# Kernel tuning notes

Hardware: AMD Instinct MI355X
Metric: run time of the kernel (lower is better)

Reference implementation:

```python
import jax, jax.numpy as jnp
import numpy as np

D_MODEL = 768
BOTTLENECK = 64
LN_EPS = 1e-5
SCALE = 1.0


def setup_inputs() -> dict:
    key = jax.random.key(0)
    k_x, k_wd = jax.random.split(key, 2)
    x = jax.random.normal(k_x, (8, 4096, D_MODEL), dtype=jnp.float32)
    # LayerNorm affine params
    ln_gamma = jnp.ones((D_MODEL,), dtype=jnp.float32)
    ln_beta = jnp.zeros((D_MODEL,), dtype=jnp.float32)
    # down_proj: kaiming_uniform_(a=sqrt(5)) -> bound = 1/sqrt(fan_in)
    bound = 1.0 / np.sqrt(D_MODEL)
    w_down = jax.random.uniform(k_wd, (D_MODEL, BOTTLENECK), dtype=jnp.float32,
                                minval=-bound, maxval=bound)
    b_down = jnp.zeros((BOTTLENECK,), dtype=jnp.float32)
    # up_proj initialized to zeros per 'lora' init; use small nonzero to make grads informative?
    # Stay faithful: zeros, as in the module's init.
    w_up = jnp.zeros((BOTTLENECK, D_MODEL), dtype=jnp.float32)
    b_up = jnp.zeros((D_MODEL,), dtype=jnp.float32)
    return {"x": x, "ln_gamma": ln_gamma, "ln_beta": ln_beta,
            "w_down": w_down, "b_down": b_down, "w_up": w_up, "b_up": b_up}


def _layer_norm(x, gamma, beta):
    mean = jnp.mean(x, axis=-1, keepdims=True)
    var = jnp.var(x, axis=-1, keepdims=True)
    return (x - mean) * jax.lax.rsqrt(var + LN_EPS) * gamma + beta


def reference(x, ln_gamma, ln_beta, w_down, b_down, w_up, b_up):
    # adapter_layernorm_option == 'in': LN before down projection
    h = _layer_norm(x, ln_gamma, ln_beta)              # [B, S, D]
    down = jnp.einsum('bsd,dk->bsk', h, w_down) + b_down  # [B, S, K]
    down = jax.nn.relu(down)
    # dropout is identity in eval mode
    out = jnp.einsum('bsk,kd->bsd', down, w_up) + b_up    # [B, S, D]
    return out * SCALE
```

## Files before the change

kernel.cpp:

```cpp
#include <hip/hip_runtime.h>
#include <hip/hip_bf16.h>


#define D_MODEL 768
#define KB      64
#define NTHR    256
#define PPAD    72

typedef __attribute__((ext_vector_type(8))) short    bf16x8;
typedef __attribute__((ext_vector_type(4))) float    f32x4;
typedef __attribute__((ext_vector_type(4))) unsigned short us4;

static __device__ __forceinline__ unsigned short f2bf(float f) {
  unsigned int u = __builtin_bit_cast(unsigned int, f);
  unsigned int r = u + 0x7FFFu + ((u >> 16) & 1u);
  return (unsigned short)(r >> 16);
}

__global__ void adapter_prep(const float* __restrict__ wd,
                             const float* __restrict__ wu,
                             const float* __restrict__ gamma,
                             const float* __restrict__ beta,
                             const float* __restrict__ bdown,
                             unsigned short* __restrict__ wdT,
                             unsigned short* __restrict__ wuT,
                             float* __restrict__ s_arr,
                             float* __restrict__ t_arr) {
  const int b = blockIdx.x;
  const int t = threadIdx.x;
  if (b < 192) {
    const int i = b * 256 + t;
    const int k1 = i / D_MODEL;
    const int d1 = i - k1 * D_MODEL;
    wdT[i] = f2bf(gamma[d1] * wd[(size_t)d1 * KB + k1]);
    const int d2 = i >> 6;
    const int k2 = i & 63;
    wuT[i] = f2bf(wu[(size_t)k2 * D_MODEL + d2]);
  } else {
    const int k = t & 63;
    const int c = t >> 6;
    float ss = 0.f, tt = 0.f;
    const int d0 = c * 192;
    #pragma unroll 4
    for (int d = d0; d < d0 + 192; ++d) {
      const float w = wd[(size_t)d * KB + k];
      ss = fmaf(gamma[d], w, ss);
      tt = fmaf(beta[d],  w, tt);
    }
    __shared__ float ps[4][64], pt[4][64];
    ps[c][k] = ss; pt[c][k] = tt;
    __syncthreads();
    if (t < 64) {
      s_arr[t] = ps[0][t] + ps[1][t] + ps[2][t] + ps[3][t];
      t_arr[t] = pt[0][t] + pt[1][t] + pt[2][t] + pt[3][t] + bdown[t];
    }
  }
}

__global__ void __launch_bounds__(NTHR, 4) adapter_main(
    const float* __restrict__ x,
    const float* __restrict__ s_arr,
    const float* __restrict__ t_arr,
    const unsigned short* __restrict__ wdT,
    const unsigned short* __restrict__ wuT,
    const float* __restrict__ b_up,
    float* __restrict__ out) {

  __shared__ unsigned short p_s[4][16][PPAD];

  const int t   = threadIdx.x;
  const int wid = t >> 6;
  const int l   = t & 63;
  const int lr  = l & 15;
  const int lg  = l >> 4;
  const int row0 = blockIdx.x * 64 + wid * 16;

  const float* xp = x + (size_t)(row0 + lr) * D_MODEL + 8 * lg;
  const unsigned short* wp = wdT + (size_t)lr * D_MODEL + 8 * lg;

  f32x4 acc0 = {0.f,0.f,0.f,0.f}, acc1 = {0.f,0.f,0.f,0.f};
  f32x4 acc2 = {0.f,0.f,0.f,0.f}, acc3 = {0.f,0.f,0.f,0.f};
  float s1 = 0.f, s2 = 0.f;

  #pragma unroll
  for (int kk = 0; kk < 24; ++kk) {
    const float4 v0 = *(const float4*)(xp + 32 * kk);
    const float4 v1 = *(const float4*)(xp + 32 * kk + 4);
    s1 += (v0.x + v0.y) + (v0.z + v0.w) + (v1.x + v1.y) + (v1.z + v1.w);
    s2 = fmaf(v0.x, v0.x, s2); s2 = fmaf(v0.y, v0.y, s2);
    s2 = fmaf(v0.z, v0.z, s2); s2 = fmaf(v0.w, v0.w, s2);
    s2 = fmaf(v1.x, v1.x, s2); s2 = fmaf(v1.y, v1.y, s2);
    s2 = fmaf(v1.z, v1.z, s2); s2 = fmaf(v1.w, v1.w, s2);
    bf16x8 xf;
    xf[0] = (short)f2bf(v0.x); xf[1] = (short)f2bf(v0.y);
    xf[2] = (short)f2bf(v0.z); xf[3] = (short)f2bf(v0.w);
    xf[4] = (short)f2bf(v1.x); xf[5] = (short)f2bf(v1.y);
    xf[6] = (short)f2bf(v1.z); xf[7] = (short)f2bf(v1.w);
    const bf16x8 wa0 = *(const bf16x8*)(wp + 32 * kk);
    const bf16x8 wa1 = *(const bf16x8*)(wp + 16 * D_MODEL + 32 * kk);
    const bf16x8 wa2 = *(const bf16x8*)(wp + 32 * D_MODEL + 32 * kk);
    const bf16x8 wa3 = *(const bf16x8*)(wp + 48 * D_MODEL + 32 * kk);
    acc0 = __builtin_amdgcn_mfma_f32_16x16x32_bf16(wa0, xf, acc0, 0, 0, 0);
    acc1 = __builtin_amdgcn_mfma_f32_16x16x32_bf16(wa1, xf, acc1, 0, 0, 0);
    acc2 = __builtin_amdgcn_mfma_f32_16x16x32_bf16(wa2, xf, acc2, 0, 0, 0);
    acc3 = __builtin_amdgcn_mfma_f32_16x16x32_bf16(wa3, xf, acc3, 0, 0, 0);
  }

  s1 += __shfl_xor(s1, 16); s1 += __shfl_xor(s1, 32);
  s2 += __shfl_xor(s2, 16); s2 += __shfl_xor(s2, 32);
  const float mu  = s1 * (1.0f / 768.0f);
  const float var = s2 * (1.0f / 768.0f) - mu * mu;
  const float rs  = rsqrtf(var + 1e-5f);
  const float nm  = -rs * mu;

  #pragma unroll
  for (int c = 0; c < 4; ++c) {
    const f32x4 a = (c == 0) ? acc0 : (c == 1) ? acc1 : (c == 2) ? acc2 : acc3;
    const float4 sv = *(const float4*)(s_arr + 16 * c + 4 * lg);
    const float4 tv = *(const float4*)(t_arr + 16 * c + 4 * lg);
    us4 pk;
    pk.x = f2bf(fmaxf(fmaf(rs, a[0], fmaf(nm, sv.x, tv.x)), 0.f));
    pk.y = f2bf(fmaxf(fmaf(rs, a[1], fmaf(nm, sv.y, tv.y)), 0.f));
    pk.z = f2bf(fmaxf(fmaf(rs, a[2], fmaf(nm, sv.z, tv.z)), 0.f));
    pk.w = f2bf(fmaxf(fmaf(rs, a[3], fmaf(nm, sv.w, tv.w)), 0.f));
    *(us4*)&p_s[wid][lr][16 * c + 4 * lg] = pk;
  }

  __syncthreads();

  const bf16x8 pa0 = *(const bf16x8*)&p_s[wid][lr][8 * lg];
  const bf16x8 pa1 = *(const bf16x8*)&p_s[wid][lr][32 + 8 * lg];
  float* op = out + (size_t)(row0 + 4 * lg) * D_MODEL + lr;

  #pragma unroll 4
  for (int n = 0; n < 48; ++n) {
    const int cn = 16 * n;
    const unsigned short* bp = wuT + (size_t)(cn + lr) * KB + 8 * lg;
    f32x4 c0 = {0.f, 0.f, 0.f, 0.f};
    c0 = __builtin_amdgcn_mfma_f32_16x16x32_bf16(pa0, *(const bf16x8*)(bp), c0, 0, 0, 0);
    c0 = __builtin_amdgcn_mfma_f32_16x16x32_bf16(pa1, *(const bf16x8*)(bp + 32), c0, 0, 0, 0);
    const float bu = b_up[cn + lr];
    op[(size_t)0 * D_MODEL + cn] = c0[0] + bu;
    op[(size_t)1 * D_MODEL + cn] = c0[1] + bu;
    op[(size_t)2 * D_MODEL + cn] = c0[2] + bu;
    op[(size_t)3 * D_MODEL + cn] = c0[3] + bu;
  }
}

extern "C" void kernel_launch(void* const* d_in, const int* in_sizes, int n_in,
                              void* d_out, int out_size, void* d_ws, size_t ws_size,
                              hipStream_t stream) {
  const float* x     = (const float*)d_in[0];
  const float* gamma = (const float*)d_in[1];
  const float* beta  = (const float*)d_in[2];
  const float* wd    = (const float*)d_in[3];
  const float* bdown = (const float*)d_in[4];
  const float* wu    = (const float*)d_in[5];
  const float* bup   = (const float*)d_in[6];
  float* out = (float*)d_out;

  char* ws = (char*)d_ws;
  unsigned short* wdT = (unsigned short*)ws;
  unsigned short* wuT = (unsigned short*)(ws + 98304);
  float* s_arr = (float*)(ws + 196608);
  float* t_arr = (float*)(ws + 196864);

  const int rows = in_sizes[0] / D_MODEL;

  adapter_prep<<<193, NTHR, 0, stream>>>(wd, wu, gamma, beta, bdown,
                                         wdT, wuT, s_arr, t_arr);
  adapter_main<<<rows / 64, NTHR, 0, stream>>>(x, s_arr, t_arr, wdT, wuT, bup, out);
}
```

Before: 224.5 us.

## Software-pipeline x and weight loads in adapter main kernel with register double buffering

The main kernel now prefetches x rows in chunks and the down-projection weight fragments two steps ahead into double-buffered registers. The up-projection weights and biases are likewise prefetched chunk by chunk, so global loads overlap with MFMA work. The unneeded block-wide __syncthreads is dropped because each wave reads only its own LDS slice. Launch bounds are relaxed to 2 waves per SIMD to make room for the extra registers, and the prep kernel is retiled to 1024-thread blocks, trading occupancy for memory-level parallelism within each wave.

```diff
diff --git a/kernel.cpp b/kernel.cpp
--- a/kernel.cpp
+++ b/kernel.cpp
@@ -7,6 +7,11 @@
 #define NTHR    256
 #define PPAD    72
 
+#define CH1     4
+#define NCH1    6
+#define CH2     6
+#define NCH2    8
+
 typedef __attribute__((ext_vector_type(8))) short    bf16x8;
 typedef __attribute__((ext_vector_type(4))) float    f32x4;
 typedef __attribute__((ext_vector_type(4))) unsigned short us4;
@@ -17,19 +22,20 @@
   return (unsigned short)(r >> 16);
 }
 
-__global__ void adapter_prep(const float* __restrict__ wd,
-                             const float* __restrict__ wu,
-                             const float* __restrict__ gamma,
-                             const float* __restrict__ beta,
-                             const float* __restrict__ bdown,
-                             unsigned short* __restrict__ wdT,
-                             unsigned short* __restrict__ wuT,
-                             float* __restrict__ s_arr,
-                             float* __restrict__ t_arr) {
+__global__ void __launch_bounds__(1024) adapter_prep(
+    const float* __restrict__ wd,
+    const float* __restrict__ wu,
+    const float* __restrict__ gamma,
+    const float* __restrict__ beta,
+    const float* __restrict__ bdown,
+    unsigned short* __restrict__ wdT,
+    unsigned short* __restrict__ wuT,
+    float* __restrict__ s_arr,
+    float* __restrict__ t_arr) {
   const int b = blockIdx.x;
   const int t = threadIdx.x;
-  if (b < 192) {
-    const int i = b * 256 + t;
+  if (b < 48) {
+    const int i = b * 1024 + t;
     const int k1 = i / D_MODEL;
     const int d1 = i - k1 * D_MODEL;
     wdT[i] = f2bf(gamma[d1] * wd[(size_t)d1 * KB + k1]);
@@ -40,24 +46,27 @@
     const int k = t & 63;
     const int c = t >> 6;
     float ss = 0.f, tt = 0.f;
-    const int d0 = c * 192;
+    const int d0 = c * 48;
     #pragma unroll 4
-    for (int d = d0; d < d0 + 192; ++d) {
+    for (int d = d0; d < d0 + 48; ++d) {
       const float w = wd[(size_t)d * KB + k];
       ss = fmaf(gamma[d], w, ss);
       tt = fmaf(beta[d],  w, tt);
     }
-    __shared__ float ps[4][64], pt[4][64];
+    __shared__ float ps[16][64], pt[16][64];
     ps[c][k] = ss; pt[c][k] = tt;
     __syncthreads();
     if (t < 64) {
-      s_arr[t] = ps[0][t] + ps[1][t] + ps[2][t] + ps[3][t];
-      t_arr[t] = pt[0][t] + pt[1][t] + pt[2][t] + pt[3][t] + bdown[t];
-    }
-  }
-}
-
-__global__ void __launch_bounds__(NTHR, 4) adapter_main(
+      float S = 0.f, T = 0.f;
+      #pragma unroll
+      for (int q = 0; q < 16; ++q) { S += ps[q][t]; T += pt[q][t]; }
+      s_arr[t] = S;
+      t_arr[t] = T + bdown[t];
+    }
+  }
+}
+
+__global__ void __launch_bounds__(NTHR, 2) adapter_main(
     const float* __restrict__ x,
     const float* __restrict__ s_arr,
     const float* __restrict__ t_arr,
@@ -78,32 +87,59 @@
   const float* xp = x + (size_t)(row0 + lr) * D_MODEL + 8 * lg;
   const unsigned short* wp = wdT + (size_t)lr * D_MODEL + 8 * lg;
 
-  f32x4 acc0 = {0.f,0.f,0.f,0.f}, acc1 = {0.f,0.f,0.f,0.f};
-  f32x4 acc2 = {0.f,0.f,0.f,0.f}, acc3 = {0.f,0.f,0.f,0.f};
+  f32x4 acc[4];
+  #pragma unroll
+  for (int c = 0; c < 4; ++c) acc[c] = (f32x4){0.f, 0.f, 0.f, 0.f};
   float s1 = 0.f, s2 = 0.f;
 
-  #pragma unroll
-  for (int kk = 0; kk < 24; ++kk) {
-    const float4 v0 = *(const float4*)(xp + 32 * kk);
-    const float4 v1 = *(const float4*)(xp + 32 * kk + 4);
-    s1 += (v0.x + v0.y) + (v0.z + v0.w) + (v1.x + v1.y) + (v1.z + v1.w);
-    s2 = fmaf(v0.x, v0.x, s2); s2 = fmaf(v0.y, v0.y, s2);
-    s2 = fmaf(v0.z, v0.z, s2); s2 = fmaf(v0.w, v0.w, s2);
-    s2 = fmaf(v1.x, v1.x, s2); s2 = fmaf(v1.y, v1.y, s2);
-    s2 = fmaf(v1.z, v1.z, s2); s2 = fmaf(v1.w, v1.w, s2);
-    bf16x8 xf;
-    xf[0] = (short)f2bf(v0.x); xf[1] = (short)f2bf(v0.y);
-    xf[2] = (short)f2bf(v0.z); xf[3] = (short)f2bf(v0.w);
-    xf[4] = (short)f2bf(v1.x); xf[5] = (short)f2bf(v1.y);
-    xf[6] = (short)f2bf(v1.z); xf[7] = (short)f2bf(v1.w);
-    const bf16x8 wa0 = *(const bf16x8*)(wp + 32 * kk);
-    const bf16x8 wa1 = *(const bf16x8*)(wp + 16 * D_MODEL + 32 * kk);
-    const bf16x8 wa2 = *(const bf16x8*)(wp + 32 * D_MODEL + 32 * kk);
-    const bf16x8 wa3 = *(const bf16x8*)(wp + 48 * D_MODEL + 32 * kk);
-    acc0 = __builtin_amdgcn_mfma_f32_16x16x32_bf16(wa0, xf, acc0, 0, 0, 0);
-    acc1 = __builtin_amdgcn_mfma_f32_16x16x32_bf16(wa1, xf, acc1, 0, 0, 0);
-    acc2 = __builtin_amdgcn_mfma_f32_16x16x32_bf16(wa2, xf, acc2, 0, 0, 0);
-    acc3 = __builtin_amdgcn_mfma_f32_16x16x32_bf16(wa3, xf, acc3, 0, 0, 0);
+  float4 xb[2][CH1][2];
+  bf16x8 wf[2][4];
+
+  #pragma unroll
+  for (int j = 0; j < CH1; ++j) {
+    xb[0][j][0] = *(const float4*)(xp + 32 * j);
+    xb[0][j][1] = *(const float4*)(xp + 32 * j + 4);
+  }
+  #pragma unroll
+  for (int c = 0; c < 4; ++c) {
+    wf[0][c] = *(const bf16x8*)(wp + (size_t)16 * c * D_MODEL);
+    wf[1][c] = *(const bf16x8*)(wp + (size_t)16 * c * D_MODEL + 32);
+  }
+
+  #pragma unroll
+  for (int ch = 0; ch < NCH1; ++ch) {
+    const int cur = ch & 1, nxt = cur ^ 1;
+    if (ch < NCH1 - 1) {
+      #pragma unroll
+      for (int j = 0; j < CH1; ++j) {
+        xb[nxt][j][0] = *(const float4*)(xp + 32 * (CH1 * (ch + 1) + j));
+        xb[nxt][j][1] = *(const float4*)(xp + 32 * (CH1 * (ch + 1) + j) + 4);
+      }
+    }
+    #pragma unroll
+    for (int j = 0; j < CH1; ++j) {
+      const int kk = CH1 * ch + j;
+      const float4 v0 = xb[cur][j][0];
+      const float4 v1 = xb[cur][j][1];
+      s1 += (v0.x + v0.y) + (v0.z + v0.w) + (v1.x + v1.y) + (v1.z + v1.w);
+      s2 = fmaf(v0.x, v0.x, s2); s2 = fmaf(v0.y, v0.y, s2);
+      s2 = fmaf(v0.z, v0.z, s2); s2 = fmaf(v0.w, v0.w, s2);
+      s2 = fmaf(v1.x, v1.x, s2); s2 = fmaf(v1.y, v1.y, s2);
+      s2 = fmaf(v1.z, v1.z, s2); s2 = fmaf(v1.w, v1.w, s2);
+      bf16x8 xf;
+      xf[0] = (short)f2bf(v0.x); xf[1] = (short)f2bf(v0.y);
+      xf[2] = (short)f2bf(v0.z); xf[3] = (short)f2bf(v0.w);
+      xf[4] = (short)f2bf(v1.x); xf[5] = (short)f2bf(v1.y);
+      xf[6] = (short)f2bf(v1.z); xf[7] = (short)f2bf(v1.w);
+      #pragma unroll
+      for (int c = 0; c < 4; ++c)
+        acc[c] = __builtin_amdgcn_mfma_f32_16x16x32_bf16(wf[kk & 1][c], xf, acc[c], 0, 0, 0);
+      if (kk + 2 < 24) {
+        #pragma unroll
+        for (int c = 0; c < 4; ++c)
+          wf[kk & 1][c] = *(const bf16x8*)(wp + (size_t)16 * c * D_MODEL + 32 * (kk + 2));
+      }
+    }
   }
 
   s1 += __shfl_xor(s1, 16); s1 += __shfl_xor(s1, 32);
@@ -115,35 +151,56 @@
 
   #pragma unroll
   for (int c = 0; c < 4; ++c) {
-    const f32x4 a = (c == 0) ? acc0 : (c == 1) ? acc1 : (c == 2) ? acc2 : acc3;
     const float4 sv = *(const float4*)(s_arr + 16 * c + 4 * lg);
     const float4 tv = *(const float4*)(t_arr + 16 * c + 4 * lg);
     us4 pk;
-    pk.x = f2bf(fmaxf(fmaf(rs, a[0], fmaf(nm, sv.x, tv.x)), 0.f));
-    pk.y = f2bf(fmaxf(fmaf(rs, a[1], fmaf(nm, sv.y, tv.y)), 0.f));
-    pk.z = f2bf(fmaxf(fmaf(rs, a[2], fmaf(nm, sv.z, tv.z)), 0.f));
-    pk.w = f2bf(fmaxf(fmaf(rs, a[3], fmaf(nm, sv.w, tv.w)), 0.f));
+    pk.x = f2bf(fmaxf(fmaf(rs, acc[c][0], fmaf(nm, sv.x, tv.x)), 0.f));
+    pk.y = f2bf(fmaxf(fmaf(rs, acc[c][1], fmaf(nm, sv.y, tv.y)), 0.f));
+    pk.z = f2bf(fmaxf(fmaf(rs, acc[c][2], fmaf(nm, sv.z, tv.z)), 0.f));
+    pk.w = f2bf(fmaxf(fmaf(rs, acc[c][3], fmaf(nm, sv.w, tv.w)), 0.f));
     *(us4*)&p_s[wid][lr][16 * c + 4 * lg] = pk;
   }
-
-  __syncthreads();
 
   const bf16x8 pa0 = *(const bf16x8*)&p_s[wid][lr][8 * lg];
   const bf16x8 pa1 = *(const bf16x8*)&p_s[wid][lr][32 + 8 * lg];
   float* op = out + (size_t)(row0 + 4 * lg) * D_MODEL + lr;
 
-  #pragma unroll 4
-  for (int n = 0; n < 48; ++n) {
-    const int cn = 16 * n;
+  bf16x8 wb[2][CH2][2];
+  float  bb[2][CH2];
+  #pragma unroll
+  for (int j = 0; j < CH2; ++j) {
+    const int cn = 16 * j;
     const unsigned short* bp = wuT + (size_t)(cn + lr) * KB + 8 * lg;
-    f32x4 c0 = {0.f, 0.f, 0.f, 0.f};
-    c0 = __builtin_amdgcn_mfma_f32_16x16x32_bf16(pa0, *(const bf16x8*)(bp), c0, 0, 0, 0);
-    c0 = __builtin_amdgcn_mfma_f32_16x16x32_bf16(pa1, *(const bf16x8*)(bp + 32), c0, 0, 0, 0);
-    const float bu = b_up[cn + lr];
-    op[(size_t)0 * D_MODEL + cn] = c0[0] + bu;
-    op[(size_t)1 * D_MODEL + cn] = c0[1] + bu;
-    op[(size_t)2 * D_MODEL + cn] = c0[2] + bu;
-    op[(size_t)3 * D_MODEL + cn] = c0[3] + bu;
+    wb[0][j][0] = *(const bf16x8*)(bp);
+    wb[0][j][1] = *(const bf16x8*)(bp + 32);
+    bb[0][j]    = b_up[cn + lr];
+  }
+
+  #pragma unroll
+  for (int ch = 0; ch < NCH2; ++ch) {
+    const int cur = ch & 1, nxt = cur ^ 1;
+    if (ch < NCH2 - 1) {
+      #pragma unroll
+      for (int j = 0; j < CH2; ++j) {
+        const int cn = 16 * (CH2 * (ch + 1) + j);
+        const unsigned short* bp = wuT + (size_t)(cn + lr) * KB + 8 * lg;
+        wb[nxt][j][0] = *(const bf16x8*)(bp);
+        wb[nxt][j][1] = *(const bf16x8*)(bp + 32);
+        bb[nxt][j]    = b_up[cn + lr];
+      }
+    }
+    #pragma unroll
+    for (int j = 0; j < CH2; ++j) {
+      const int cn = 16 * (CH2 * ch + j);
+      f32x4 c0 = {0.f, 0.f, 0.f, 0.f};
+      c0 = __builtin_amdgcn_mfma_f32_16x16x32_bf16(pa0, wb[cur][j][0], c0, 0, 0, 0);
+      c0 = __builtin_amdgcn_mfma_f32_16x16x32_bf16(pa1, wb[cur][j][1], c0, 0, 0, 0);
+      const float bu = bb[cur][j];
+      op[(size_t)0 * D_MODEL + cn] = c0[0] + bu;
+      op[(size_t)1 * D_MODEL + cn] = c0[1] + bu;
+      op[(size_t)2 * D_MODEL + cn] = c0[2] + bu;
+      op[(size_t)3 * D_MODEL + cn] = c0[3] + bu;
+    }
   }
 }
 
@@ -167,7 +224,7 @@
 
   const int rows = in_sizes[0] / D_MODEL;
 
-  adapter_prep<<<193, NTHR, 0, stream>>>(wd, wu, gamma, beta, bdown,
-                                         wdT, wuT, s_arr, t_arr);
+  adapter_prep<<<49, 1024, 0, stream>>>(wd, wu, gamma, beta, bdown,
+                                        wdT, wuT, s_arr, t_arr);
   adapter_main<<<rows / 64, NTHR, 0, stream>>>(x, s_arr, t_arr, wdT, wuT, bup, out);
 }
```

Measured after the change: 221.9 us. Within noise of the previous version (-1.2%).

## Split LN-GEMM K dimension across wave pairs and halve rows per block

Applied to the files above, without the earlier changes.

Each 16-row tile is now processed by two waves, each handling half of the 768-wide reduction. Partial LayerNorm statistics and MFMA accumulators are exchanged through shared memory, and each wave then handles half of the up-projection output columns. The x loads are batched into register arrays ahead of the compute, and the prep kernel uses 1024-thread blocks. The goal is more blocks and more memory-level parallelism for the bandwidth-bound stream over x, at the cost of an extra LDS exchange and a block-wide barrier.

```diff
diff --git a/kernel.cpp b/kernel.cpp
--- a/kernel.cpp
+++ b/kernel.cpp
@@ -17,19 +17,29 @@
   return (unsigned short)(r >> 16);
 }
 
-__global__ void adapter_prep(const float* __restrict__ wd,
-                             const float* __restrict__ wu,
-                             const float* __restrict__ gamma,
-                             const float* __restrict__ beta,
-                             const float* __restrict__ bdown,
-                             unsigned short* __restrict__ wdT,
-                             unsigned short* __restrict__ wuT,
-                             float* __restrict__ s_arr,
-                             float* __restrict__ t_arr) {
+static __device__ __forceinline__ bf16x8 pack_bf8(const f32x4 a, const f32x4 b) {
+  union { __hip_bfloat162 h2[4]; bf16x8 v; } u;
+  u.h2[0] = __float22bfloat162_rn({a[0], a[1]});
+  u.h2[1] = __float22bfloat162_rn({a[2], a[3]});
+  u.h2[2] = __float22bfloat162_rn({b[0], b[1]});
+  u.h2[3] = __float22bfloat162_rn({b[2], b[3]});
+  return u.v;
+}
+
+__global__ void __launch_bounds__(1024) adapter_prep(
+    const float* __restrict__ wd,
+    const float* __restrict__ wu,
+    const float* __restrict__ gamma,
+    const float* __restrict__ beta,
+    const float* __restrict__ bdown,
+    unsigned short* __restrict__ wdT,
+    unsigned short* __restrict__ wuT,
+    float* __restrict__ s_arr,
+    float* __restrict__ t_arr) {
   const int b = blockIdx.x;
   const int t = threadIdx.x;
-  if (b < 192) {
-    const int i = b * 256 + t;
+  if (b < 48) {
+    const int i = b * 1024 + t;
     const int k1 = i / D_MODEL;
     const int d1 = i - k1 * D_MODEL;
     wdT[i] = f2bf(gamma[d1] * wd[(size_t)d1 * KB + k1]);
@@ -40,19 +50,22 @@
     const int k = t & 63;
     const int c = t >> 6;
     float ss = 0.f, tt = 0.f;
-    const int d0 = c * 192;
+    const int d0 = c * 48;
     #pragma unroll 4
-    for (int d = d0; d < d0 + 192; ++d) {
+    for (int d = d0; d < d0 + 48; ++d) {
       const float w = wd[(size_t)d * KB + k];
       ss = fmaf(gamma[d], w, ss);
       tt = fmaf(beta[d],  w, tt);
     }
-    __shared__ float ps[4][64], pt[4][64];
+    __shared__ float ps[16][64], pt[16][64];
     ps[c][k] = ss; pt[c][k] = tt;
     __syncthreads();
     if (t < 64) {
-      s_arr[t] = ps[0][t] + ps[1][t] + ps[2][t] + ps[3][t];
-      t_arr[t] = pt[0][t] + pt[1][t] + pt[2][t] + pt[3][t] + bdown[t];
+      float S = 0.f, T = 0.f;
+      #pragma unroll
+      for (int q = 0; q < 16; ++q) { S += ps[q][t]; T += pt[q][t]; }
+      s_arr[t] = S;
+      t_arr[t] = T + bdown[t];
     }
   }
 }
@@ -66,46 +79,69 @@
     const float* __restrict__ b_up,
     float* __restrict__ out) {
 
-  __shared__ unsigned short p_s[4][16][PPAD];
-
-  const int t   = threadIdx.x;
-  const int wid = t >> 6;
-  const int l   = t & 63;
-  const int lr  = l & 15;
-  const int lg  = l >> 4;
-  const int row0 = blockIdx.x * 64 + wid * 16;
-
-  const float* xp = x + (size_t)(row0 + lr) * D_MODEL + 8 * lg;
-  const unsigned short* wp = wdT + (size_t)lr * D_MODEL + 8 * lg;
+  __shared__ float sst[4][64][2];
+  __shared__ __align__(16) float aex[4][2][64][4];
+  __shared__ unsigned short p_s[2][16][PPAD];
+
+  const int t  = threadIdx.x;
+  const int w  = t >> 6;
+  const int l  = t & 63;
+  const int lr = l & 15;
+  const int lg = l >> 4;
+  const int rt = w >> 1;
+  const int kh = w & 1;
+  const int rb = blockIdx.x * 32 + 16 * rt;
+
+  const float* xp = x + (size_t)(rb + lr) * D_MODEL + 384 * kh + 8 * lg;
+  const unsigned short* wp = wdT + (size_t)lr * D_MODEL + 384 * kh + 8 * lg;
 
   f32x4 acc0 = {0.f,0.f,0.f,0.f}, acc1 = {0.f,0.f,0.f,0.f};
   f32x4 acc2 = {0.f,0.f,0.f,0.f}, acc3 = {0.f,0.f,0.f,0.f};
   float s1 = 0.f, s2 = 0.f;
 
   #pragma unroll
-  for (int kk = 0; kk < 24; ++kk) {
-    const float4 v0 = *(const float4*)(xp + 32 * kk);
-    const float4 v1 = *(const float4*)(xp + 32 * kk + 4);
-    s1 += (v0.x + v0.y) + (v0.z + v0.w) + (v1.x + v1.y) + (v1.z + v1.w);
-    s2 = fmaf(v0.x, v0.x, s2); s2 = fmaf(v0.y, v0.y, s2);
-    s2 = fmaf(v0.z, v0.z, s2); s2 = fmaf(v0.w, v0.w, s2);
-    s2 = fmaf(v1.x, v1.x, s2); s2 = fmaf(v1.y, v1.y, s2);
-    s2 = fmaf(v1.z, v1.z, s2); s2 = fmaf(v1.w, v1.w, s2);
-    bf16x8 xf;
-    xf[0] = (short)f2bf(v0.x); xf[1] = (short)f2bf(v0.y);
-    xf[2] = (short)f2bf(v0.z); xf[3] = (short)f2bf(v0.w);
-    xf[4] = (short)f2bf(v1.x); xf[5] = (short)f2bf(v1.y);
-    xf[6] = (short)f2bf(v1.z); xf[7] = (short)f2bf(v1.w);
-    const bf16x8 wa0 = *(const bf16x8*)(wp + 32 * kk);
-    const bf16x8 wa1 = *(const bf16x8*)(wp + 16 * D_MODEL + 32 * kk);
-    const bf16x8 wa2 = *(const bf16x8*)(wp + 32 * D_MODEL + 32 * kk);
-    const bf16x8 wa3 = *(const bf16x8*)(wp + 48 * D_MODEL + 32 * kk);
-    acc0 = __builtin_amdgcn_mfma_f32_16x16x32_bf16(wa0, xf, acc0, 0, 0, 0);
-    acc1 = __builtin_amdgcn_mfma_f32_16x16x32_bf16(wa1, xf, acc1, 0, 0, 0);
-    acc2 = __builtin_amdgcn_mfma_f32_16x16x32_bf16(wa2, xf, acc2, 0, 0, 0);
-    acc3 = __builtin_amdgcn_mfma_f32_16x16x32_bf16(wa3, xf, acc3, 0, 0, 0);
-  }
-
+  for (int half = 0; half < 2; ++half) {
+    f32x4 xv[6][2];
+    #pragma unroll
+    for (int j = 0; j < 6; ++j) {
+      const float* p = xp + 32 * (6 * half + j);
+      xv[j][0] = *(const f32x4*)(p);
+      xv[j][1] = *(const f32x4*)(p + 4);
+    }
+    asm volatile("" ::: "memory");
+    #pragma unroll
+    for (int j = 0; j < 6; ++j) {
+      const int kkl = 6 * half + j;
+      const f32x4 v0 = xv[j][0];
+      const f32x4 v1 = xv[j][1];
+      s1 += (v0[0] + v0[1]) + (v0[2] + v0[3]) + (v1[0] + v1[1]) + (v1[2] + v1[3]);
+      s2 = fmaf(v0[0], v0[0], s2); s2 = fmaf(v0[1], v0[1], s2);
+      s2 = fmaf(v0[2], v0[2], s2); s2 = fmaf(v0[3], v0[3], s2);
+      s2 = fmaf(v1[0], v1[0], s2); s2 = fmaf(v1[1], v1[1], s2);
+      s2 = fmaf(v1[2], v1[2], s2); s2 = fmaf(v1[3], v1[3], s2);
+      const bf16x8 xf = pack_bf8(v0, v1);
+      const unsigned short* wq = wp + 32 * kkl;
+      acc0 = __builtin_amdgcn_mfma_f32_16x16x32_bf16(*(const bf16x8*)(wq),                    xf, acc0, 0, 0, 0);
+      acc1 = __builtin_amdgcn_mfma_f32_16x16x32_bf16(*(const bf16x8*)(wq + 16 * D_MODEL),     xf, acc1, 0, 0, 0);
+      acc2 = __builtin_amdgcn_mfma_f32_16x16x32_bf16(*(const bf16x8*)(wq + 32 * D_MODEL),     xf, acc2, 0, 0, 0);
+      acc3 = __builtin_amdgcn_mfma_f32_16x16x32_bf16(*(const bf16x8*)(wq + 48 * D_MODEL),     xf, acc3, 0, 0, 0);
+    }
+  }
+
+  sst[w][l][0] = s1;
+  sst[w][l][1] = s2;
+  if (kh == 0) {
+    *(f32x4*)aex[w][0][l] = acc2;
+    *(f32x4*)aex[w][1][l] = acc3;
+  } else {
+    *(f32x4*)aex[w][0][l] = acc0;
+    *(f32x4*)aex[w][1][l] = acc1;
+  }
+  __syncthreads();
+
+  const int pw = w ^ 1;
+  s1 += sst[pw][l][0];
+  s2 += sst[pw][l][1];
   s1 += __shfl_xor(s1, 16); s1 += __shfl_xor(s1, 32);
   s2 += __shfl_xor(s2, 16); s2 += __shfl_xor(s2, 32);
   const float mu  = s1 * (1.0f / 768.0f);
@@ -113,31 +149,38 @@
   const float rs  = rsqrtf(var + 1e-5f);
   const float nm  = -rs * mu;
 
+  const f32x4 pe0 = *(const f32x4*)aex[pw][0][l];
+  const f32x4 pe1 = *(const f32x4*)aex[pw][1][l];
+  f32x4 f0, f1; int cbase;
+  if (kh == 0) { f0 = acc0 + pe0; f1 = acc1 + pe1; cbase = 0; }
+  else         { f0 = acc2 + pe0; f1 = acc3 + pe1; cbase = 2; }
+
   #pragma unroll
-  for (int c = 0; c < 4; ++c) {
-    const f32x4 a = (c == 0) ? acc0 : (c == 1) ? acc1 : (c == 2) ? acc2 : acc3;
-    const float4 sv = *(const float4*)(s_arr + 16 * c + 4 * lg);
-    const float4 tv = *(const float4*)(t_arr + 16 * c + 4 * lg);
+  for (int i = 0; i < 2; ++i) {
+    const f32x4 a = i ? f1 : f0;
+    const int co = cbase + i;
+    const float4 sv = *(const float4*)(s_arr + 16 * co + 4 * lg);
+    const float4 tv = *(const float4*)(t_arr + 16 * co + 4 * lg);
     us4 pk;
     pk.x = f2bf(fmaxf(fmaf(rs, a[0], fmaf(nm, sv.x, tv.x)), 0.f));
     pk.y = f2bf(fmaxf(fmaf(rs, a[1], fmaf(nm, sv.y, tv.y)), 0.f));
     pk.z = f2bf(fmaxf(fmaf(rs, a[2], fmaf(nm, sv.z, tv.z)), 0.f));
     pk.w = f2bf(fmaxf(fmaf(rs, a[3], fmaf(nm, sv.w, tv.w)), 0.f));
-    *(us4*)&p_s[wid][lr][16 * c + 4 * lg] = pk;
-  }
-
+    *(us4*)&p_s[rt][lr][16 * co + 4 * lg] = pk;
+  }
   __syncthreads();
 
-  const bf16x8 pa0 = *(const bf16x8*)&p_s[wid][lr][8 * lg];
-  const bf16x8 pa1 = *(const bf16x8*)&p_s[wid][lr][32 + 8 * lg];
-  float* op = out + (size_t)(row0 + 4 * lg) * D_MODEL + lr;
-
-  #pragma unroll 4
-  for (int n = 0; n < 48; ++n) {
-    const int cn = 16 * n;
+  const bf16x8 pa0 = *(const bf16x8*)&p_s[rt][lr][8 * lg];
+  const bf16x8 pa1 = *(const bf16x8*)&p_s[rt][lr][32 + 8 * lg];
+  float* op = out + (size_t)(rb + 4 * lg) * D_MODEL + lr;
+  const int n0 = 24 * kh;
+
+  #pragma unroll 6
+  for (int i = 0; i < 24; ++i) {
+    const int cn = 16 * (n0 + i);
     const unsigned short* bp = wuT + (size_t)(cn + lr) * KB + 8 * lg;
     f32x4 c0 = {0.f, 0.f, 0.f, 0.f};
-    c0 = __builtin_amdgcn_mfma_f32_16x16x32_bf16(pa0, *(const bf16x8*)(bp), c0, 0, 0, 0);
+    c0 = __builtin_amdgcn_mfma_f32_16x16x32_bf16(pa0, *(const bf16x8*)(bp),      c0, 0, 0, 0);
     c0 = __builtin_amdgcn_mfma_f32_16x16x32_bf16(pa1, *(const bf16x8*)(bp + 32), c0, 0, 0, 0);
     const float bu = b_up[cn + lr];
     op[(size_t)0 * D_MODEL + cn] = c0[0] + bu;
@@ -167,7 +210,7 @@
 
   const int rows = in_sizes[0] / D_MODEL;
 
-  adapter_prep<<<193, NTHR, 0, stream>>>(wd, wu, gamma, beta, bdown,
-                                         wdT, wuT, s_arr, t_arr);
-  adapter_main<<<rows / 64, NTHR, 0, stream>>>(x, s_arr, t_arr, wdT, wuT, bup, out);
-}
+  adapter_prep<<<49, 1024, 0, stream>>>(wd, wu, gamma, beta, bdown,
+                                        wdT, wuT, s_arr, t_arr);
+  adapter_main<<<rows / 32, NTHR, 0, stream>>>(x, s_arr, t_arr, wdT, wuT, bup, out);
+}
```

Result: no change. 221.1 us (-1.6%).
